# Kernel optimization log

Hardware: AMD Instinct MI355X
Metric: run time of the kernel (lower is better)

The kernel has to match this reference:

```python
import jax, jax.numpy as jnp
import numpy as np

NUM_HEADS = 16

def _rope_tables(seq_len, dim, dtype):
    # LongLlamaRotaryEmbedding: inv_freq = 1/10000^(2i/d), emb = cat(freqs, freqs)
    inv_freq = 1.0 / (10000.0 ** (jnp.arange(0, dim, 2, dtype=jnp.float32) / dim))
    t = jnp.arange(seq_len, dtype=jnp.float32)
    freqs = t[:, None] * inv_freq[None, :]            # [S, D/2]
    emb = jnp.concatenate([freqs, freqs], axis=-1)    # [S, D]
    return jnp.cos(emb).astype(dtype), jnp.sin(emb).astype(dtype)

def _rotate_half(x):
    x1, x2 = jnp.split(x, 2, axis=-1)
    return jnp.concatenate([-x2, x1], axis=-1)

def _rotate_one(x, cos, sin, pos):
    # x: [B,H,S,D]; pos: [B,S] int -> gather-indexed RoPE
    c = cos[pos][:, None, :, :]  # [B,1,S,D]
    s = sin[pos][:, None, :, :]
    return x * c + _rotate_half(x) * s

def setup_inputs() -> dict:
    key = jax.random.key(0)
    B, S, HID = 1, 4096, 2048
    ks = jax.random.split(key, 5)
    hidden_states = jax.random.normal(ks[0], (B, S, HID), dtype=jnp.float32)
    # causal additive mask [B,1,S,S]: 0 where allowed, large negative above diagonal
    causal = jnp.tril(jnp.ones((S, S), dtype=bool))
    attention_mask = jnp.where(causal, 0.0, -1e9).astype(jnp.float32)[None, None]
    attention_mask = jnp.broadcast_to(attention_mask, (B, 1, S, S))
    position_ids = jnp.broadcast_to(jnp.arange(S, dtype=jnp.int64), (B, S))
    scale = 0.02
    Wq = jax.random.normal(ks[1], (HID, HID), dtype=jnp.float32) * scale
    Wk = jax.random.normal(ks[2], (HID, HID), dtype=jnp.float32) * scale
    Wv = jax.random.normal(ks[3], (HID, HID), dtype=jnp.float32) * scale
    Wo = jax.random.normal(ks[4], (HID, HID), dtype=jnp.float32) * scale
    return {"hidden_states": hidden_states, "attention_mask": attention_mask,
            "position_ids": position_ids, "Wq": Wq, "Wk": Wk, "Wv": Wv, "Wo": Wo}

def reference(hidden_states, attention_mask, position_ids, Wq, Wk, Wv, Wo):
    B, S, HID = hidden_states.shape
    H = NUM_HEADS
    D = HID // H
    # QKV projections (torch Linear: y = x @ W.T), shaped [B,H,S,D]
    q = (hidden_states @ Wq.T).reshape(B, S, H, D).transpose(0, 2, 1, 3)
    k = (hidden_states @ Wk.T).reshape(B, S, H, D).transpose(0, 2, 1, 3)
    v = (hidden_states @ Wv.T).reshape(B, S, H, D).transpose(0, 2, 1, 3)
    kv_seq_len = k.shape[-2]
    cos, sin = _rope_tables(kv_seq_len, D, hidden_states.dtype)
    # rel_pos_ids = position_ids - min over seq (gather-indexed RoPE)
    rel = position_ids - jnp.min(position_ids, axis=-1, keepdims=True)
    q = _rotate_one(q, cos, sin, rel[:, -S:])
    k = _rotate_one(k, cos, sin, rel)
    scores = jnp.einsum('bhqd,bhkd->bhqk', q, k) / jnp.asarray(np.sqrt(D), hidden_states.dtype)
    scores = scores + attention_mask  # additive mask broadcast over heads
    attn = jax.nn.softmax(scores, axis=-1)
    out = jnp.einsum('bhqk,bhkd->bhqd', attn, v)
    out = out.transpose(0, 2, 1, 3).reshape(B, S, HID)
    return out @ Wo.T
```

## Files before the change

### kernel.cpp

```cpp
#include <hip/hip_runtime.h>
#include <stdint.h>

typedef uint16_t u16;
typedef __bf16 bf16x8 __attribute__((ext_vector_type(8)));
typedef float f32x4 __attribute__((ext_vector_type(4)));
typedef uint32_t u32x4 __attribute__((ext_vector_type(4)));

__device__ __forceinline__ u16 f2bf(float f) {
    uint32_t u = __builtin_bit_cast(uint32_t, f);
    u += 0x7fffu + ((u >> 16) & 1u);
    return (u16)(u >> 16);
}
__device__ __forceinline__ float bf2f(u16 h) {
    uint32_t u = ((uint32_t)h) << 16;
    return __builtin_bit_cast(float, u);
}

__global__ __launch_bounds__(256) void cvt_f32_bf16(const float* __restrict__ in,
                                                    u16* __restrict__ out, int n4) {
    int i = blockIdx.x * 256 + threadIdx.x;
    if (i >= n4) return;
    float4 v = ((const float4*)in)[i];
    u16 o[4] = { f2bf(v.x), f2bf(v.y), f2bf(v.z), f2bf(v.w) };
    *(uint64_t*)(out + 4 * (size_t)i) = *(const uint64_t*)o;
}

__device__ __forceinline__ void gload16(const u16* g, u16* l) {
    __builtin_amdgcn_global_load_lds(
        (const __attribute__((address_space(1))) void*)g,
        (__attribute__((address_space(3))) void*)l, 16, 0, 0);
}

__global__ __launch_bounds__(256) void gemm_qkv(const u16* __restrict__ A,
                                                const u16* __restrict__ B,
                                                u16* __restrict__ C0,
                                                u16* __restrict__ C1,
                                                u16* __restrict__ C2,
                                                int K) {
    __shared__ u16 As[128 * 32];
    __shared__ u16 Bs[128 * 32];
    const int tid  = threadIdx.x;
    const int wave = tid >> 6, lane = tid & 63;
    const int quad = lane >> 4, ln = lane & 15;
    const int bm = blockIdx.x, bn = blockIdx.y;
    const int wm = (wave & 1) * 64, wn = (wave >> 1) * 64;
    const u16* Ab = A + (size_t)bm * 128 * K;
    const u16* Bb = B + (size_t)bn * 128 * K;
    const int r0 = tid >> 2, g0 = (tid & 3) * 8;
    const int r1 = 64 + r0;
    u16* AsW0 = As + wave * 512;
    u16* AsW1 = As + 2048 + wave * 512;
    u16* BsW0 = Bs + wave * 512;
    u16* BsW1 = Bs + 2048 + wave * 512;

    f32x4 acc[4][4] = {};
    for (int k0 = 0; k0 < K; k0 += 32) {
        gload16(Ab + (size_t)r0 * K + k0 + g0, AsW0);
        gload16(Ab + (size_t)r1 * K + k0 + g0, AsW1);
        gload16(Bb + (size_t)r0 * K + k0 + g0, BsW0);
        gload16(Bb + (size_t)r1 * K + k0 + g0, BsW1);
        __syncthreads();
        bf16x8 a[4], b[4];
#pragma unroll
        for (int i = 0; i < 4; i++) {
            a[i] = *(const bf16x8*)(As + (wm + i * 16 + ln) * 32 + quad * 8);
            b[i] = *(const bf16x8*)(Bs + (wn + i * 16 + ln) * 32 + quad * 8);
        }
#pragma unroll
        for (int i = 0; i < 4; i++)
#pragma unroll
            for (int j = 0; j < 4; j++)
                acc[i][j] = __builtin_amdgcn_mfma_f32_16x16x32_bf16(a[i], b[j], acc[i][j], 0, 0, 0);
        __syncthreads();
    }
    u16* outB = (bn < 16 ? C0 : (bn < 32 ? C1 : C2));
#pragma unroll
    for (int i = 0; i < 4; i++)
#pragma unroll
        for (int j = 0; j < 4; j++)
#pragma unroll
            for (int r = 0; r < 4; r++) {
                size_t row = (size_t)(bm * 128 + wm + i * 16 + quad * 4 + r);
                int coll = (bn & 15) * 128 + wn + j * 16 + ln;
                outB[row * 2048 + coll] = f2bf(acc[i][j][r]);
            }
}

__global__ __launch_bounds__(256) void gemm_bt64(const u16* __restrict__ A,
                                                 const u16* __restrict__ B,
                                                 float* __restrict__ C,
                                                 int M, int N, int K) {
    __shared__ u16 As[64 * 32];
    __shared__ u16 Bs[128 * 32];
    const int tid  = threadIdx.x;
    const int wave = tid >> 6, lane = tid & 63;
    const int quad = lane >> 4, ln = lane & 15;
    const int bm = blockIdx.x, bn = blockIdx.y;
    const int wm = (wave & 1) * 32, wn = (wave >> 1) * 64;
    const u16* Ab = A + (size_t)bm * 64 * K;
    const u16* Bb = B + (size_t)bn * 128 * K;
    const int pa = wave * 64 + lane, ra = pa >> 2, ga = (pa & 3) * 8;

    f32x4 acc[2][4] = {};
    for (int k0 = 0; k0 < K; k0 += 32) {
        gload16(Ab + (size_t)ra * K + k0 + ga, As + wave * 512);
#pragma unroll
        for (int t = 0; t < 2; t++) {
            int p = (wave * 2 + t) * 64 + lane;
            int r = p >> 2, g = (p & 3) * 8;
            gload16(Bb + (size_t)r * K + k0 + g, Bs + (wave * 2 + t) * 512);
        }
        __syncthreads();
        bf16x8 a[2], b[4];
#pragma unroll
        for (int i = 0; i < 2; i++)
            a[i] = *(const bf16x8*)(As + (wm + i * 16 + ln) * 32 + quad * 8);
#pragma unroll
        for (int j = 0; j < 4; j++)
            b[j] = *(const bf16x8*)(Bs + (wn + j * 16 + ln) * 32 + quad * 8);
#pragma unroll
        for (int i = 0; i < 2; i++)
#pragma unroll
            for (int j = 0; j < 4; j++)
                acc[i][j] = __builtin_amdgcn_mfma_f32_16x16x32_bf16(a[i], b[j], acc[i][j], 0, 0, 0);
        __syncthreads();
    }
#pragma unroll
    for (int i = 0; i < 2; i++)
#pragma unroll
        for (int j = 0; j < 4; j++)
#pragma unroll
            for (int r = 0; r < 4; r++) {
                size_t row = (size_t)(bm * 64 + wm + i * 16 + quad * 4 + r);
                size_t col = (size_t)(bn * 128 + wn + j * 16 + ln);
                C[row * N + col] = acc[i][j][r];
            }
}

__global__ __launch_bounds__(256) void rope_scale(u16* __restrict__ Qb,
                                                  u16* __restrict__ Kb) {
    int idx = blockIdx.x * 256 + threadIdx.x;
    int s   = idx >> 11;
    int rem = idx & 2047;
    int mat = rem >> 10;
    int h   = (rem >> 6) & 15;
    int j   = rem & 63;
    u16* base = (mat ? Kb : Qb) + (size_t)s * 2048 + h * 128;
    float x1 = bf2f(base[j]);
    float x2 = bf2f(base[j + 64]);
    float invf = exp2f((float)(-j) * 0.2076205059304601f);
    float th = (float)s * invf;
    float sn, cs;
    sincosf(th, &sn, &cs);
    float o1 = x1 * cs - x2 * sn;
    float o2 = x2 * cs + x1 * sn;
    const float QS = 0.08838834764831845f * 1.4426950408889634f;
    if (mat == 0) { o1 *= QS; o2 *= QS; }
    base[j]      = f2bf(o1);
    base[j + 64] = f2bf(o2);
}

__global__ __launch_bounds__(256) void transpose_v(const u16* __restrict__ V,
                                                   u16* __restrict__ Vt) {
    const int h  = blockIdx.y;
    const int s0 = blockIdx.x * 64;
    const int tid = threadIdx.x;
    for (int c = tid; c < 1024; c += 256) {
        int d = c >> 3, sc = c & 7;
        u16 tmp[8];
#pragma unroll
        for (int j = 0; j < 8; j++)
            tmp[j] = V[(size_t)(s0 + sc * 8 + j) * 2048 + h * 128 + d];
        *(u32x4*)(Vt + ((size_t)h * 128 + d) * 4096 + s0 + sc * 8) = *(const u32x4*)tmp;
    }
}

__global__ __launch_bounds__(256, 3) void fattn(const u16* __restrict__ Qb,
                                                const u16* __restrict__ Kb,
                                                const u16* __restrict__ Vt,
                                                float* __restrict__ Oacc,
                                                float* __restrict__ Lacc) {
    __shared__ u16 Ks[2][32 * 128];
    __shared__ u16 Vs[2][128 * 32];
    __shared__ u16 Ps[128][40];
    const int tid  = threadIdx.x, wave = tid >> 6, lane = tid & 63;
    const int quad = lane >> 4, ln = lane & 15;
    const int h = blockIdx.x;
    const int y = blockIdx.y;
    int c, qt;
    if (y < 32)      { c = 0; qt = 31 - y; }
    else if (y < 56) { c = 1; qt = 63 - y; }
    else if (y < 72) { c = 2; qt = 87 - y; }
    else             { c = 3; qt = 103 - y; }
    const int q0 = qt * 128;
    const int nkt = min(32, 4 * qt + 4 - 32 * c);
    const int ktbase = 32 * c;

    const u16* Kp0 = Kb + h * 128;
    const u16* Vp0 = Vt + (size_t)h * 128 * 4096;

    bf16x8 aq[2][4];
    const u16* Qp = Qb + (size_t)q0 * 2048 + h * 128;
#pragma unroll
    for (int i = 0; i < 2; i++)
#pragma unroll
        for (int ks = 0; ks < 4; ks++)
            aq[i][ks] = *(const bf16x8*)(Qp + (size_t)(wave * 32 + i * 16 + ln) * 2048
                                         + ks * 32 + quad * 8);

    f32x4 o[2][8] = {};
    float lreg[2][4] = {};

    auto stage = [&](int kt, int b) {
        const u16* Kp = Kp0 + (size_t)(kt * 32) * 2048;
        const u16* Vp = Vp0 + kt * 32;
#pragma unroll
        for (int t = 0; t < 2; t++) {
            int p = (wave * 2 + t) * 64 + lane;
            int r = p >> 4, jc = (p & 15) ^ (r & 15);
            gload16(Kp + (size_t)r * 2048 + jc * 8, &Ks[b][(wave * 2 + t) * 512]);
        }
#pragma unroll
        for (int t = 0; t < 2; t++) {
            int p = (wave * 2 + t) * 64 + lane;
            int r = p >> 2, jc = (p & 3) ^ (r & 3);
            gload16(Vp + (size_t)r * 4096 + jc * 8, &Vs[b][(wave * 2 + t) * 512]);
        }
    };

    stage(ktbase, 0);
    for (int t = 0; t < nkt; t++) {
        __syncthreads();
        if (t + 1 < nkt) stage(ktbase + t + 1, (t + 1) & 1);
        const u16* Ksb = Ks[t & 1];
        const u16* Vsb = Vs[t & 1];

        f32x4 sc[2][2] = {};
#pragma unroll
        for (int ks = 0; ks < 4; ks++)
#pragma unroll
            for (int j = 0; j < 2; j++) {
                int r = j * 16 + ln;
                bf16x8 bk = *(const bf16x8*)(Ksb + (size_t)(r * 16 + ((ks * 4 + quad) ^ ln)) * 8);
                sc[0][j] = __builtin_amdgcn_mfma_f32_16x16x32_bf16(aq[0][ks], bk, sc[0][j], 0, 0, 0);
                sc[1][j] = __builtin_amdgcn_mfma_f32_16x16x32_bf16(aq[1][ks], bk, sc[1][j], 0, 0, 0);
            }
        const int kv0 = (ktbase + t) * 32;
        if (kv0 + 31 > q0 + wave * 32) {
#pragma unroll
            for (int j = 0; j < 2; j++) {
                int col = kv0 + j * 16 + ln;
#pragma unroll
                for (int i = 0; i < 2; i++)
#pragma unroll
                    for (int r = 0; r < 4; r++) {
                        int row = q0 + wave * 32 + i * 16 + quad * 4 + r;
                        if (col > row) sc[i][j][r] = -1e30f;
                    }
            }
        }
#pragma unroll
        for (int i = 0; i < 2; i++)
#pragma unroll
            for (int r = 0; r < 4; r++) {
                float p0 = __builtin_amdgcn_exp2f(sc[i][0][r]);
                float p1 = __builtin_amdgcn_exp2f(sc[i][1][r]);
                lreg[i][r] += p0 + p1;
                int row = wave * 32 + i * 16 + quad * 4 + r;
                Ps[row][ln]      = f2bf(p0);
                Ps[row][16 + ln] = f2bf(p1);
            }
        bf16x8 pa0 = *(const bf16x8*)&Ps[wave * 32 + ln][quad * 8];
        bf16x8 pa1 = *(const bf16x8*)&Ps[wave * 32 + 16 + ln][quad * 8];
#pragma unroll
        for (int n = 0; n < 8; n++) {
            int rv = n * 16 + ln;
            bf16x8 vb = *(const bf16x8*)(Vsb + (size_t)(rv * 4 + (quad ^ (ln & 3))) * 8);
            o[0][n] = __builtin_amdgcn_mfma_f32_16x16x32_bf16(pa0, vb, o[0][n], 0, 0, 0);
            o[1][n] = __builtin_amdgcn_mfma_f32_16x16x32_bf16(pa1, vb, o[1][n], 0, 0, 0);
        }
    }
    float* Op = Oacc + (size_t)(q0 + wave * 32) * 2048 + h * 128;
#pragma unroll
    for (int i = 0; i < 2; i++)
#pragma unroll
        for (int r = 0; r < 4; r++) {
            float l = lreg[i][r];
            l += __shfl_xor(l, 1);
            l += __shfl_xor(l, 2);
            l += __shfl_xor(l, 4);
            l += __shfl_xor(l, 8);
            int row = i * 16 + quad * 4 + r;
            if (ln == 0)
                unsafeAtomicAdd(&Lacc[(size_t)(q0 + wave * 32 + row) * 16 + h], l);
#pragma unroll
            for (int n = 0; n < 8; n++)
                unsafeAtomicAdd(&Op[(size_t)row * 2048 + n * 16 + ln], o[i][n][r]);
        }
}

__global__ __launch_bounds__(256) void attn_norm(const float* __restrict__ Oacc,
                                                 const float* __restrict__ Lacc,
                                                 u16* __restrict__ attn) {
    int i = blockIdx.x * 256 + threadIdx.x;
    int s  = i >> 9;
    int c4 = (i & 511) * 4;
    int h  = c4 >> 7;
    float inv = 1.0f / Lacc[(size_t)s * 16 + h];
    float4 v = ((const float4*)(Oacc + (size_t)s * 2048))[i & 511];
    u16 o[4] = { f2bf(v.x * inv), f2bf(v.y * inv), f2bf(v.z * inv), f2bf(v.w * inv) };
    *(uint64_t*)(attn + (size_t)s * 2048 + c4) = *(const uint64_t*)o;
}

extern "C" void kernel_launch(void* const* d_in, const int* in_sizes, int n_in,
                              void* d_out, int out_size, void* d_ws, size_t ws_size,
                              hipStream_t stream) {
    const float* hs = (const float*)d_in[0];
    const float* Wq = (const float*)d_in[3];
    const float* Wk = (const float*)d_in[4];
    const float* Wv = (const float*)d_in[5];
    const float* Wo = (const float*)d_in[6];

    char* ws = (char*)d_ws;
    u16* Xb   = (u16*)ws;
    u16* Wob  = (u16*)(ws + (size_t)16777216);
    u16* Qb   = (u16*)(ws + (size_t)25165824);
    u16* Kb   = (u16*)(ws + (size_t)41943040);
    u16* Vtg  = (u16*)(ws + (size_t)58720256);
    u16* Wqkv = (u16*)(ws + (size_t)75497472);
    u16* Vb   = (u16*)(ws + (size_t)100663296);
    float* Oacc = (float*)(ws + (size_t)75497472);
    float* Lacc = (float*)(ws + (size_t)109051904);
    u16* attn = Xb;

    cvt_f32_bf16<<<8192, 256, 0, stream>>>(hs, Xb, 2097152);
    cvt_f32_bf16<<<4096, 256, 0, stream>>>(Wq, Wqkv,            1048576);
    cvt_f32_bf16<<<4096, 256, 0, stream>>>(Wk, Wqkv + 4194304,  1048576);
    cvt_f32_bf16<<<4096, 256, 0, stream>>>(Wv, Wqkv + 8388608,  1048576);
    cvt_f32_bf16<<<4096, 256, 0, stream>>>(Wo, Wob,             1048576);

    gemm_qkv<<<dim3(32, 48), 256, 0, stream>>>(Xb, Wqkv, Qb, Kb, Vb, 2048);
    rope_scale<<<32768, 256, 0, stream>>>(Qb, Kb);
    transpose_v<<<dim3(64, 16), 256, 0, stream>>>(Vb, Vtg);
    hipMemsetAsync(Oacc, 0, 33816576, stream);
    fattn<<<dim3(16, 80), 256, 0, stream>>>(Qb, Kb, Vtg, Oacc, Lacc);
    attn_norm<<<8192, 256, 0, stream>>>(Oacc, Lacc, attn);
    gemm_bt64<<<dim3(64, 16), 256, 0, stream>>>(attn, Wob, (float*)d_out, 4096, 2048, 2048);
}
```

Before: 538.1 us.

## Rewrite QKV GEMM with 256x192 tiles, double-buffered LDS and interleaved MFMA

Replaces the 128x128 QKV GEMM with a 512-thread, 256x192-tile kernel. It uses K=64 steps with double-buffered, XOR-swizzled LDS staging and interleaves global-to-LDS loads with MFMA phases using barriers and s_setprio. Output goes to Q/K/V laid out contiguously, and workspace buffers are reshuffled so V sits right after K. The aim is to hide memory latency and raise data reuse per tile. The cost is heavy LDS use and register pressure, which limits occupancy to one block per CU.

```diff
diff --git a/kernel.cpp b/kernel.cpp
--- a/kernel.cpp
+++ b/kernel.cpp
@@ -31,59 +31,115 @@
         (__attribute__((address_space(3))) void*)l, 16, 0, 0);
 }
 
-__global__ __launch_bounds__(256) void gemm_qkv(const u16* __restrict__ A,
-                                                const u16* __restrict__ B,
-                                                u16* __restrict__ C0,
-                                                u16* __restrict__ C1,
-                                                u16* __restrict__ C2,
-                                                int K) {
-    __shared__ u16 As[128 * 32];
-    __shared__ u16 Bs[128 * 32];
+__global__ __launch_bounds__(512, 1) void gemm_qkv(const u16* __restrict__ A,
+                                                   const u16* __restrict__ B,
+                                                   u16* __restrict__ Cq,
+                                                   int K) {
+    __shared__ u16 As[2][16384];
+    __shared__ u16 Bs[2][12288];
     const int tid  = threadIdx.x;
     const int wave = tid >> 6, lane = tid & 63;
     const int quad = lane >> 4, ln = lane & 15;
+    const int wm = wave >> 2, wn = wave & 3;
     const int bm = blockIdx.x, bn = blockIdx.y;
-    const int wm = (wave & 1) * 64, wn = (wave >> 1) * 64;
-    const u16* Ab = A + (size_t)bm * 128 * K;
-    const u16* Bb = B + (size_t)bn * 128 * K;
-    const int r0 = tid >> 2, g0 = (tid & 3) * 8;
-    const int r1 = 64 + r0;
-    u16* AsW0 = As + wave * 512;
-    u16* AsW1 = As + 2048 + wave * 512;
-    u16* BsW0 = Bs + wave * 512;
-    u16* BsW1 = Bs + 2048 + wave * 512;
-
-    f32x4 acc[4][4] = {};
-    for (int k0 = 0; k0 < K; k0 += 32) {
-        gload16(Ab + (size_t)r0 * K + k0 + g0, AsW0);
-        gload16(Ab + (size_t)r1 * K + k0 + g0, AsW1);
-        gload16(Bb + (size_t)r0 * K + k0 + g0, BsW0);
-        gload16(Bb + (size_t)r1 * K + k0 + g0, BsW1);
-        __syncthreads();
-        bf16x8 a[4], b[4];
-#pragma unroll
-        for (int i = 0; i < 4; i++) {
-            a[i] = *(const bf16x8*)(As + (wm + i * 16 + ln) * 32 + quad * 8);
-            b[i] = *(const bf16x8*)(Bs + (wn + i * 16 + ln) * 32 + quad * 8);
-        }
+    const int NT = K >> 6;
+    const u16* Ab = A + (size_t)bm * 256 * K;
+    const u16* Bb = B + (size_t)bn * 192 * K;
+    const int lr  = lane >> 3;
+    const int lc8 = ((lane & 7) ^ lr) * 8;
+    const int sw  = ln & 7;
+    const int cA0 = ((0 + quad) ^ sw) * 8;
+    const int cA1 = ((4 + quad) ^ sw) * 8;
+
+    f32x4 acc[8][3] = {};
+
+    auto stage_a = [&](int t, int q) {
+        int ch = q * 8 + wave;
+        gload16(Ab + (size_t)(ch * 8 + lr) * K + t * 64 + lc8, &As[t & 1][ch * 512]);
+    };
+    auto stage_b = [&](int t, int q) {
+        int ch = q * 8 + wave;
+        gload16(Bb + (size_t)(ch * 8 + lr) * K + t * 64 + lc8, &Bs[t & 1][ch * 512]);
+    };
+
+    for (int q = 0; q < 4; q++) stage_a(0, q);
+    for (int q = 0; q < 3; q++) stage_b(0, q);
+    for (int q = 0; q < 4; q++) stage_a(1, q);
+    asm volatile("s_waitcnt vmcnt(4)" ::: "memory");
+    __builtin_amdgcn_s_barrier();
+
+    for (int t = 0; t < NT; ++t) {
+        const u16* Asb = As[t & 1];
+        const u16* Bsb = Bs[t & 1];
+        bf16x8 a0[8], a1[8], b0[3], b1[3];
+#pragma unroll
+        for (int i = 0; i < 8; i++)
+            a0[i] = *(const bf16x8*)(Asb + (wm * 128 + i * 16 + ln) * 64 + cA0);
+#pragma unroll
+        for (int j = 0; j < 3; j++)
+            b0[j] = *(const bf16x8*)(Bsb + (wn * 48 + j * 16 + ln) * 64 + cA0);
+        if (t + 1 < NT) { stage_b(t + 1, 0); stage_b(t + 1, 1); }
+        __builtin_amdgcn_s_barrier();
+        asm volatile("s_waitcnt lgkmcnt(0)" ::: "memory");
+        __builtin_amdgcn_s_setprio(1);
 #pragma unroll
         for (int i = 0; i < 4; i++)
 #pragma unroll
-            for (int j = 0; j < 4; j++)
-                acc[i][j] = __builtin_amdgcn_mfma_f32_16x16x32_bf16(a[i], b[j], acc[i][j], 0, 0, 0);
-        __syncthreads();
+            for (int j = 0; j < 3; j++)
+                acc[i][j] = __builtin_amdgcn_mfma_f32_16x16x32_bf16(a0[i], b0[j], acc[i][j], 0, 0, 0);
+        __builtin_amdgcn_s_setprio(0);
+        __builtin_amdgcn_s_barrier();
+#pragma unroll
+        for (int i = 0; i < 8; i++)
+            a1[i] = *(const bf16x8*)(Asb + (wm * 128 + i * 16 + ln) * 64 + cA1);
+#pragma unroll
+        for (int j = 0; j < 3; j++)
+            b1[j] = *(const bf16x8*)(Bsb + (wn * 48 + j * 16 + ln) * 64 + cA1);
+        if (t + 1 < NT) stage_b(t + 1, 2);
+        __builtin_amdgcn_s_barrier();
+        asm volatile("s_waitcnt lgkmcnt(0)" ::: "memory");
+        __builtin_amdgcn_s_setprio(1);
+#pragma unroll
+        for (int i = 4; i < 8; i++)
+#pragma unroll
+            for (int j = 0; j < 3; j++)
+                acc[i][j] = __builtin_amdgcn_mfma_f32_16x16x32_bf16(a0[i], b0[j], acc[i][j], 0, 0, 0);
+        __builtin_amdgcn_s_setprio(0);
+        __builtin_amdgcn_s_barrier();
+        if (t + 2 < NT) { stage_a(t + 2, 0); stage_a(t + 2, 1); }
+        __builtin_amdgcn_s_barrier();
+        __builtin_amdgcn_s_setprio(1);
+#pragma unroll
+        for (int i = 0; i < 4; i++)
+#pragma unroll
+            for (int j = 0; j < 3; j++)
+                acc[i][j] = __builtin_amdgcn_mfma_f32_16x16x32_bf16(a1[i], b1[j], acc[i][j], 0, 0, 0);
+        __builtin_amdgcn_s_setprio(0);
+        __builtin_amdgcn_s_barrier();
+        if (t + 2 < NT) { stage_a(t + 2, 2); stage_a(t + 2, 3); }
+        __builtin_amdgcn_s_barrier();
+        __builtin_amdgcn_s_setprio(1);
+#pragma unroll
+        for (int i = 4; i < 8; i++)
+#pragma unroll
+            for (int j = 0; j < 3; j++)
+                acc[i][j] = __builtin_amdgcn_mfma_f32_16x16x32_bf16(a1[i], b1[j], acc[i][j], 0, 0, 0);
+        __builtin_amdgcn_s_setprio(0);
+        asm volatile("s_waitcnt vmcnt(4)" ::: "memory");
+        __builtin_amdgcn_s_barrier();
     }
-    u16* outB = (bn < 16 ? C0 : (bn < 32 ? C1 : C2));
-#pragma unroll
-    for (int i = 0; i < 4; i++)
-#pragma unroll
-        for (int j = 0; j < 4; j++)
-#pragma unroll
-            for (int r = 0; r < 4; r++) {
-                size_t row = (size_t)(bm * 128 + wm + i * 16 + quad * 4 + r);
-                int coll = (bn & 15) * 128 + wn + j * 16 + ln;
-                outB[row * 2048 + coll] = f2bf(acc[i][j][r]);
-            }
+#pragma unroll
+    for (int i = 0; i < 8; i++) {
+        size_t row0 = (size_t)(bm * 256 + wm * 128 + i * 16 + quad * 4);
+#pragma unroll
+        for (int j = 0; j < 3; j++) {
+            int n = bn * 192 + wn * 48 + j * 16 + ln;
+            size_t off = ((size_t)(n >> 11) << 23) + (size_t)(n & 2047);
+#pragma unroll
+            for (int r = 0; r < 4; r++)
+                Cq[off + (row0 + r) * 2048] = f2bf(acc[i][j][r]);
+        }
+    }
 }
 
 __global__ __launch_bounds__(256) void gemm_bt64(const u16* __restrict__ A,
@@ -326,11 +382,11 @@
     u16* Wob  = (u16*)(ws + (size_t)16777216);
     u16* Qb   = (u16*)(ws + (size_t)25165824);
     u16* Kb   = (u16*)(ws + (size_t)41943040);
-    u16* Vtg  = (u16*)(ws + (size_t)58720256);
+    u16* Vb   = (u16*)(ws + (size_t)58720256);
     u16* Wqkv = (u16*)(ws + (size_t)75497472);
-    u16* Vb   = (u16*)(ws + (size_t)100663296);
-    float* Oacc = (float*)(ws + (size_t)75497472);
-    float* Lacc = (float*)(ws + (size_t)109051904);
+    u16* Vtg  = (u16*)(ws + (size_t)100663296);
+    float* Oacc = (float*)(ws + (size_t)58720256);
+    float* Lacc = (float*)(ws + (size_t)92274688);
     u16* attn = Xb;
 
     cvt_f32_bf16<<<8192, 256, 0, stream>>>(hs, Xb, 2097152);
@@ -339,7 +395,7 @@
     cvt_f32_bf16<<<4096, 256, 0, stream>>>(Wv, Wqkv + 8388608,  1048576);
     cvt_f32_bf16<<<4096, 256, 0, stream>>>(Wo, Wob,             1048576);
 
-    gemm_qkv<<<dim3(32, 48), 256, 0, stream>>>(Xb, Wqkv, Qb, Kb, Vb, 2048);
+    gemm_qkv<<<dim3(16, 32), 512, 0, stream>>>(Xb, Wqkv, Qb, 2048);
     rope_scale<<<32768, 256, 0, stream>>>(Qb, Kb);
     transpose_v<<<dim3(64, 16), 256, 0, stream>>>(Vb, Vtg);
     hipMemsetAsync(Oacc, 0, 33816576, stream);
```

New measurement: 513.8 us. 1.05x faster.
